# Optimization experiments

Hardware: AMD Instinct MI355X
Metric: run time of the kernel (lower is better)

## Reference

```python
import jax, jax.numpy as jnp
import numpy as np

B, C, P, L = 128, 5, 5, 5
D = 128
USER_NUM, TITLE_NUM, ENTITY_NUM, REL_NUM = 50000, 30000, 100000, 100


def setup_inputs() -> dict:
    key = jax.random.key(0)
    k = jax.random.split(key, 22)
    f = jnp.float32
    s = 0.1  # weight scale to keep LSTM gates in a sane range
    return {
        "candidate_newsindex": jax.random.randint(k[0], (B, C), 0, TITLE_NUM),
        "user_index": jax.random.randint(k[1], (B,), 0, USER_NUM),
        "total_paths_index": jax.random.randint(k[2], (USER_NUM, C, P, L), 0, TITLE_NUM),
        "total_type_index": jax.random.randint(k[3], (USER_NUM, C, P, L), 0, 3),
        "total_relations_index": jax.random.randint(k[4], (USER_NUM, C, P, L), 0, REL_NUM),
        "entity_emb": jax.random.normal(k[5], (ENTITY_NUM, D), f),
        "relation_emb": jax.random.normal(k[6], (REL_NUM, D), f),
        "user_emb": jax.random.normal(k[7], (USER_NUM, D), f),
        "news_emb": jax.random.normal(k[8], (TITLE_NUM, D), f),
        "type_emb": jax.random.normal(k[9], (3, D), f),
        "Wih0": jax.random.normal(k[10], (P, 4 * D, 3 * D), f) * s,
        "Whh0": jax.random.normal(k[11], (P, 4 * D, D), f) * s,
        "bih0": jax.random.normal(k[12], (P, 4 * D), f) * s,
        "bhh0": jax.random.normal(k[13], (P, 4 * D), f) * s,
        "Wih1": jax.random.normal(k[14], (P, 4 * D, D), f) * s,
        "Whh1": jax.random.normal(k[15], (P, 4 * D, D), f) * s,
        "bih1": jax.random.normal(k[16], (P, 4 * D), f) * s,
        "bhh1": jax.random.normal(k[17], (P, 4 * D), f) * s,
        "W1": jax.random.normal(k[18], (16, D), f) * s,
        "b1": jax.random.normal(k[19], (16,), f) * s,
        "W2": jax.random.normal(k[20], (1, 16), f) * s,
        "b2": jax.random.normal(k[21], (1,), f) * s,
    }


def _lstm2(x, Wih0, Whh0, bih0, bhh0, Wih1, Whh1, bih1, bhh1):
    """2-layer PyTorch-style LSTM (gate order i,f,g,o). x: [N, T, in] -> [N, T, H]."""
    def layer(x, Wih, Whh, bih, bhh):
        N = x.shape[0]
        H = Whh.shape[1]
        h0 = jnp.zeros((N, H), x.dtype)
        c0 = jnp.zeros((N, H), x.dtype)
        b = bih + bhh
        def step(carry, xt):
            h, c = carry
            g = xt @ Wih.T + h @ Whh.T + b
            i, f, gg, o = jnp.split(g, 4, axis=-1)
            c = jax.nn.sigmoid(f) * c + jax.nn.sigmoid(i) * jnp.tanh(gg)
            h = jax.nn.sigmoid(o) * jnp.tanh(c)
            return (h, c), h
        _, ys = jax.lax.scan(step, (h0, c0), x.swapaxes(0, 1))
        return ys.swapaxes(0, 1)
    x = layer(x, Wih0, Whh0, bih0, bhh0)
    x = layer(x, Wih1, Whh1, bih1, bhh1)
    return x


def reference(candidate_newsindex, user_index, total_paths_index, total_type_index,
              total_relations_index, entity_emb, relation_emb, user_emb, news_emb,
              type_emb, Wih0, Whh0, bih0, bhh0, Wih1, Whh1, bih1, bhh1,
              W1, b1, W2, b2):
    bpath = total_paths_index[user_index]  # [B,C,P,L]
    btype = total_type_index[user_index]
    brel = total_relations_index[user_index]
    # per-node embedding selected by type: 0->user, 1->news, else entity
    node = jnp.where((btype == 0)[..., None], user_emb[bpath],
                     jnp.where((btype == 1)[..., None], news_emb[bpath], entity_emb[bpath]))
    inp = jnp.concatenate([node, type_emb[btype], relation_emb[brel]], axis=-1)  # [B,C,P,L,3D]
    Bb, Cc, Pp, Ll, F = inp.shape
    x = inp.transpose(2, 0, 1, 3, 4).reshape(Pp, Bb * Cc, Ll, F)  # per-path batches
    outs = jax.vmap(_lstm2)(x, Wih0, Whh0, bih0, bhh0, Wih1, Whh1, bih1, bhh1)  # [P,BC,L,H]
    idx = jnp.arange(Pp)
    sel = outs[idx, :, idx, :]  # LSTM i's output at timestep i -> [P, BC, H]
    ps = jax.nn.sigmoid(jnp.maximum(sel @ W1.T + b1, 0.0) @ W2.T + b2)[..., 0]  # [P,BC]
    ps_mean = ps.reshape(Pp, Bb, Cc).mean(axis=0)  # [B,C]
    # faithful to source: total_output accumulates over candidates j, so the score
    # for candidate j is the cumulative mean of path scores for candidates 0..j
    total_score = jnp.cumsum(ps_mean, axis=1) / jnp.arange(1, Cc + 1, dtype=ps_mean.dtype)
    emb_score = jax.nn.sigmoid(jnp.sum(news_emb[candidate_newsindex] * user_emb[user_index][:, None, :], axis=-1))
    return emb_score + total_score
```

## Files before the change

kernel.cpp:

```cpp
#include <hip/hip_runtime.h>
#include <math.h>

#define BB   128
#define CC   5
#define PP   5
#define LL   5
#define DD   128
#define NSEQ 640
#define GATES 512
#define IN0  384
#define GSW  516
#define HPAD 136

typedef __attribute__((ext_vector_type(8))) short short8;
typedef __attribute__((ext_vector_type(4))) float f32x4;

__device__ __forceinline__ float sigf(float x){ return 1.0f/(1.0f+__expf(-x)); }
__device__ __forceinline__ float tanhfast(float x){ return 1.0f - 2.0f/(__expf(2.0f*x)+1.0f); }

__device__ __forceinline__ unsigned short f2bf(float x){
    union { float f; unsigned u; } v; v.f = x;
    unsigned r = v.u + 0x7FFF + ((v.u >> 16) & 1);
    return (unsigned short)(r >> 16);
}

__global__ void prep_kernel(const float* __restrict__ Wih0, const float* __restrict__ Whh0,
                            const float* __restrict__ Wih1, const float* __restrict__ Whh1,
                            const float* __restrict__ bih0, const float* __restrict__ bhh0,
                            const float* __restrict__ bih1, const float* __restrict__ bhh1,
                            unsigned short* __restrict__ F0, unsigned short* __restrict__ F1,
                            unsigned short* __restrict__ F2, unsigned short* __restrict__ F3,
                            float* __restrict__ b0, float* __restrict__ b1c){
    int id = blockIdx.x*256 + threadIdx.x;
    const int NF0 = PP*12*32*64;
    const int NFH = PP*4*32*64;
    if (id < NF0 + 3*NFH){
        const float* src; unsigned short* dst; int K, KT, fid;
        if (id < NF0){ src = Wih0; dst = F0; K = IN0; KT = 12; fid = id; }
        else {
            int j = id - NF0; int m = j / NFH; fid = j % NFH; K = DD; KT = 4;
            src = (m==0)?Whh0:(m==1)?Wih1:Whh1;
            dst = (m==0)?F1:(m==1)?F2:F3;
        }
        int lane = fid & 63; int rem = fid >> 6;
        int gt = rem & 31; rem >>= 5;
        int kt = rem % KT; int p = rem / KT;
        int g  = gt*16 + (lane & 15);
        int k0 = kt*32 + (lane >> 4)*8;
        const float* s = src + (size_t)(p*GATES + g)*K + k0;
        float4 x0 = *(const float4*)s;
        float4 x1 = *(const float4*)(s+4);
        uint4 o;
        o.x = f2bf(x0.x) | ((unsigned)f2bf(x0.y)<<16);
        o.y = f2bf(x0.z) | ((unsigned)f2bf(x0.w)<<16);
        o.z = f2bf(x1.x) | ((unsigned)f2bf(x1.y)<<16);
        o.w = f2bf(x1.z) | ((unsigned)f2bf(x1.w)<<16);
        *(uint4*)(dst + (size_t)fid*8) = o;
    } else {
        int j = id - (NF0 + 3*NFH);
        if (j < PP*GATES) b0[j] = bih0[j] + bhh0[j];
        else if (j < 2*PP*GATES){ int q = j - PP*GATES; b1c[q] = bih1[q] + bhh1[q]; }
    }
}

__global__ void gather_x(const int* __restrict__ user_index,
                         const int* __restrict__ tpath, const int* __restrict__ ttype,
                         const int* __restrict__ trel,
                         const float* __restrict__ entity_emb, const float* __restrict__ relation_emb,
                         const float* __restrict__ user_emb, const float* __restrict__ news_emb,
                         const float* __restrict__ type_emb,
                         unsigned short* __restrict__ X){
    int id = blockIdx.x*256 + threadIdx.x;
    if (id >= PP*LL*NSEQ*48) return;
    int pt = id / (NSEQ*48); int rem = id % (NSEQ*48);
    int n = rem / 48, q = rem % 48;
    int p = pt / LL, t = pt % LL;
    if (t > p) return;
    int b = n / CC, c = n % CC;
    int u = user_index[b];
    int base = ((u*CC + c)*PP + p)*LL + t;
    int col = q*8;
    const float* s;
    if (q < 16){
        int ty = ttype[base]; int pi = tpath[base];
        const float* e = (ty==0)?user_emb:(ty==1)?news_emb:entity_emb;
        s = e + (size_t)pi*DD + col;
    } else if (q < 32){
        s = type_emb + (size_t)ttype[base]*DD + (col-128);
    } else {
        s = relation_emb + (size_t)trel[base]*DD + (col-256);
    }
    float4 x0 = *(const float4*)s, x1 = *(const float4*)(s+4);
    uint4 o;
    o.x = f2bf(x0.x) | ((unsigned)f2bf(x0.y)<<16);
    o.y = f2bf(x0.z) | ((unsigned)f2bf(x0.w)<<16);
    o.z = f2bf(x1.x) | ((unsigned)f2bf(x1.y)<<16);
    o.w = f2bf(x1.z) | ((unsigned)f2bf(x1.w)<<16);
    *(uint4*)(X + (size_t)(pt*NSEQ + n)*IN0 + col) = o;
}

__global__ __launch_bounds__(256) void gemm_ih0_v3(const unsigned short* __restrict__ X,
                                                   const unsigned short* __restrict__ F0,
                                                   float* __restrict__ G0c){
    __shared__ unsigned short Bs[12*4*512];
    int bx = blockIdx.x;
    int nch = bx & 7;
    int m64 = (bx >> 3) % 10;
    int pt  = bx / 80;
    int p = pt / LL, t = pt % LL;
    if (t > p) return;
    int tid = threadIdx.x, lane = tid & 63, w = tid >> 6;
    int r16 = lane & 15, qd = lane >> 4;

    const unsigned short* Fp = F0 + (((size_t)p*12)*32 + nch*4)*512;
    uint4 breg[12];
    #pragma unroll
    for (int j=0;j<12;j++)
        breg[j] = *(const uint4*)(Fp + (size_t)j*32*512 + tid*8);
    #pragma unroll
    for (int j=0;j<12;j++)
        *(uint4*)(Bs + j*2048 + tid*8) = breg[j];
    __syncthreads();

    f32x4 acc[4];
    #pragma unroll
    for (int i=0;i<4;i++) acc[i] = (f32x4)0.0f;
    const unsigned short* Xb = X + ((size_t)pt*NSEQ + m64*64 + w*16 + r16)*IN0 + qd*8;
    #pragma unroll
    for (int kt=0; kt<12; kt++){
        short8 a = *(const short8*)(Xb + kt*32);
        #pragma unroll
        for (int i=0;i<4;i++){
            short8 bfr = *(const short8*)(Bs + (kt*4+i)*512 + lane*8);
            acc[i] = __builtin_amdgcn_mfma_f32_16x16x32_bf16(a, bfr, acc[i], 0,0,0);
        }
    }
    int tile16 = pt*40 + m64*4 + w;
    float* dst = G0c + (((size_t)tile16*32 + nch*4)*64 + lane)*4;
    #pragma unroll
    for (int i=0;i<4;i++)
        *(f32x4*)(dst + (size_t)i*256) = acc[i];
}

__global__ __launch_bounds__(512) void lstm_v3(
    const float* __restrict__ G0c,
    const unsigned short* __restrict__ F1,
    const unsigned short* __restrict__ F2,
    const unsigned short* __restrict__ F3,
    const float* __restrict__ b0, const float* __restrict__ b1c,
    const float* __restrict__ W1, const float* __restrict__ b1v,
    const float* __restrict__ W2, const float* __restrict__ b2v,
    float* __restrict__ psum){
    __shared__ float GS[16*GSW];
    __shared__ unsigned short h0T[16*HPAD];
    __shared__ unsigned short h1T[16*HPAD];
    __shared__ float h1f[16*132];
    __shared__ float mlpb[16*17];

    int p = blockIdx.x / 40, nt = blockIdx.x % 40;
    int n0 = nt*16;
    int tid = threadIdx.x;
    int lane = tid & 63, w = tid >> 6;
    int r16 = lane & 15, qd = lane >> 4;
    int cr = tid >> 5, cj = (tid & 31)*4;

    for (int i = tid; i < 16*HPAD/2; i += 512){
        ((unsigned*)h0T)[i] = 0u; ((unsigned*)h1T)[i] = 0u;
    }

    short8 f2r[16], f3r[16];
    {
        const unsigned short* F2p = F2 + (size_t)p*4*32*512 + lane*8;
        const unsigned short* F3p = F3 + (size_t)p*4*32*512 + lane*8;
        #pragma unroll
        for (int kt=0; kt<4; kt++)
            #pragma unroll
            for (int i=0;i<4;i++){
                f2r[kt*4+i] = *(const short8*)(F2p + (size_t)(kt*32 + w*4+i)*512);
                f3r[kt*4+i] = *(const short8*)(F3p + (size_t)(kt*32 + w*4+i)*512);
            }
    }
    float bL0[4], bL1[4];
    #pragma unroll
    for (int i=0;i<4;i++){
        int col = (w*4+i)*16 + r16;
        bL0[i] = b0[p*GATES + col];
        bL1[i] = b1c[p*GATES + col];
    }
    const unsigned short* F1p = F1 + (size_t)p*4*32*512 + lane*8;

    f32x4 pf[4];
    {
        const float* slab = G0c + (size_t)((p*LL + 0)*40 + nt)*8192;
        #pragma unroll
        for (int i=0;i<4;i++) pf[i] = *(const f32x4*)(slab + ((w*4+i)*64 + lane)*4);
    }
    float c0s[4] = {0,0,0,0}, c1s[4] = {0,0,0,0};
    __syncthreads();

    for (int t=0; t<=p; t++){
        f32x4 acc[4];
        #pragma unroll
        for (int i=0;i<4;i++){
            f32x4 a = pf[i]; float bb = bL0[i];
            a[0]+=bb; a[1]+=bb; a[2]+=bb; a[3]+=bb;
            acc[i] = a;
        }
        if (t < p){
            const float* ns = G0c + (size_t)((p*LL + t + 1)*40 + nt)*8192;
            #pragma unroll
            for (int i=0;i<4;i++) pf[i] = *(const f32x4*)(ns + ((w*4+i)*64 + lane)*4);
        }
        if (t > 0){
            #pragma unroll
            for (int kt=0; kt<4; kt++){
                short8 a = *(const short8*)(h0T + r16*HPAD + kt*32 + qd*8);
                #pragma unroll
                for (int i=0;i<4;i++){
                    short8 bfr = *(const short8*)(F1p + (size_t)(kt*32 + w*4+i)*512);
                    acc[i] = __builtin_amdgcn_mfma_f32_16x16x32_bf16(a, bfr, acc[i], 0,0,0);
                }
            }
        }
        #pragma unroll
        for (int i=0;i<4;i++)
            #pragma unroll
            for (int v=0;v<4;v++)
                GS[(qd*4+v)*GSW + (w*4+i)*16 + r16] = acc[i][v];
        __syncthreads();
        {
            const float* gsr = GS + cr*GSW;
            float4 gi = *(const float4*)(gsr + cj);
            float4 gf = *(const float4*)(gsr + 128 + cj);
            float4 gg = *(const float4*)(gsr + 256 + cj);
            float4 go = *(const float4*)(gsr + 384 + cj);
            float hv[4];
            const float* pi = (const float*)&gi; const float* pfv = (const float*)&gf;
            const float* pg = (const float*)&gg; const float* po = (const float*)&go;
            #pragma unroll
            for (int s=0;s<4;s++){
                float cc = sigf(pfv[s])*c0s[s] + sigf(pi[s])*tanhfast(pg[s]);
                c0s[s] = cc;
                hv[s] = sigf(po[s])*tanhfast(cc);
            }
            uint2 pk;
            pk.x = f2bf(hv[0]) | ((unsigned)f2bf(hv[1])<<16);
            pk.y = f2bf(hv[2]) | ((unsigned)f2bf(hv[3])<<16);
            *(uint2*)(h0T + cr*HPAD + cj) = pk;
        }
        __syncthreads();
        #pragma unroll
        for (int i=0;i<4;i++){
            float bb = bL1[i];
            f32x4 a; a[0]=bb; a[1]=bb; a[2]=bb; a[3]=bb;
            acc[i] = a;
        }
        #pragma unroll
        for (int kt=0; kt<4; kt++){
            short8 a = *(const short8*)(h0T + r16*HPAD + kt*32 + qd*8);
            #pragma unroll
            for (int i=0;i<4;i++)
                acc[i] = __builtin_amdgcn_mfma_f32_16x16x32_bf16(a, f2r[kt*4+i], acc[i], 0,0,0);
        }
        if (t > 0){
            #pragma unroll
            for (int kt=0; kt<4; kt++){
                short8 a = *(const short8*)(h1T + r16*HPAD + kt*32 + qd*8);
                #pragma unroll
                for (int i=0;i<4;i++)
                    acc[i] = __builtin_amdgcn_mfma_f32_16x16x32_bf16(a, f3r[kt*4+i], acc[i], 0,0,0);
            }
        }
        #pragma unroll
        for (int i=0;i<4;i++)
            #pragma unroll
            for (int v=0;v<4;v++)
                GS[(qd*4+v)*GSW + (w*4+i)*16 + r16] = acc[i][v];
        __syncthreads();
        {
            const float* gsr = GS + cr*GSW;
            float4 gi = *(const float4*)(gsr + cj);
            float4 gf = *(const float4*)(gsr + 128 + cj);
            float4 gg = *(const float4*)(gsr + 256 + cj);
            float4 go = *(const float4*)(gsr + 384 + cj);
            float hv[4];
            const float* pi = (const float*)&gi; const float* pfv = (const float*)&gf;
            const float* pg = (const float*)&gg; const float* po = (const float*)&go;
            #pragma unroll
            for (int s=0;s<4;s++){
                float cc = sigf(pfv[s])*c1s[s] + sigf(pi[s])*tanhfast(pg[s]);
                c1s[s] = cc;
                hv[s] = sigf(po[s])*tanhfast(cc);
            }
            if (t < p){
                uint2 pk;
                pk.x = f2bf(hv[0]) | ((unsigned)f2bf(hv[1])<<16);
                pk.y = f2bf(hv[2]) | ((unsigned)f2bf(hv[3])<<16);
                *(uint2*)(h1T + cr*HPAD + cj) = pk;
            } else {
                float4 st; st.x=hv[0]; st.y=hv[1]; st.z=hv[2]; st.w=hv[3];
                *(float4*)(h1f + cr*132 + cj) = st;
            }
        }
        __syncthreads();
    }
    if (tid < 256){
        int rr = tid & 15, hc = tid >> 4;
        const float* w1r = W1 + hc*DD;
        float acc = b1v[hc];
        #pragma unroll 4
        for (int k=0;k<DD;k++) acc = fmaf(h1f[rr*132 + k], w1r[k], acc);
        mlpb[hc*17 + rr] = fmaxf(acc, 0.0f);
    }
    __syncthreads();
    if (tid < 16){
        float s = b2v[0];
        #pragma unroll
        for (int h=0;h<16;h++) s = fmaf(mlpb[h*17 + tid], W2[h], s);
        atomicAdd(&psum[n0 + tid], 0.2f*sigf(s));
    }
}

__global__ void final_kernel(const int* __restrict__ cand, const int* __restrict__ user_index,
                             const float* __restrict__ news_emb, const float* __restrict__ user_emb,
                             const float* __restrict__ psum, float* __restrict__ out){
    int b = blockIdx.x;
    int lane = threadIdx.x;
    int u = user_index[b];
    const float* ue = user_emb + (size_t)u*DD;
    float cum = 0.0f;
    for (int c=0;c<CC;c++){
        int nb = cand[b*CC + c];
        const float* ne = news_emb + (size_t)nb*DD;
        float v = ne[lane]*ue[lane] + ne[lane+64]*ue[lane+64];
        #pragma unroll
        for (int off=32; off; off>>=1) v += __shfl_down(v, off, 64);
        if (lane == 0){
            cum += psum[b*CC + c];
            out[b*CC + c] = sigf(v) + cum/(float)(c+1);
        }
    }
}

extern "C" void kernel_launch(void* const* d_in, const int* in_sizes, int n_in,
                              void* d_out, int out_size, void* d_ws, size_t ws_size,
                              hipStream_t stream){
    const int* cand        = (const int*)d_in[0];
    const int* uidx        = (const int*)d_in[1];
    const int* tpath       = (const int*)d_in[2];
    const int* ttype       = (const int*)d_in[3];
    const int* trel        = (const int*)d_in[4];
    const float* entity_emb   = (const float*)d_in[5];
    const float* relation_emb = (const float*)d_in[6];
    const float* user_emb     = (const float*)d_in[7];
    const float* news_emb     = (const float*)d_in[8];
    const float* type_emb     = (const float*)d_in[9];
    const float* Wih0 = (const float*)d_in[10];
    const float* Whh0 = (const float*)d_in[11];
    const float* bih0 = (const float*)d_in[12];
    const float* bhh0 = (const float*)d_in[13];
    const float* Wih1 = (const float*)d_in[14];
    const float* Whh1 = (const float*)d_in[15];
    const float* bih1 = (const float*)d_in[16];
    const float* bhh1 = (const float*)d_in[17];
    const float* W1 = (const float*)d_in[18];
    const float* b1 = (const float*)d_in[19];
    const float* W2 = (const float*)d_in[20];
    const float* b2 = (const float*)d_in[21];
    float* out = (float*)d_out;

    char* ws = (char*)d_ws;
    unsigned short* F0 = (unsigned short*)ws;  ws += (size_t)PP*12*32*512*2;
    unsigned short* F1 = (unsigned short*)ws;  ws += (size_t)PP*4*32*512*2;
    unsigned short* F2 = (unsigned short*)ws;  ws += (size_t)PP*4*32*512*2;
    unsigned short* F3 = (unsigned short*)ws;  ws += (size_t)PP*4*32*512*2;
    float* b0  = (float*)ws;                   ws += PP*GATES*4;
    float* b1c = (float*)ws;                   ws += PP*GATES*4;
    unsigned short* X = (unsigned short*)ws;   ws += (size_t)PP*LL*NSEQ*IN0*2;
    float* G0c = (float*)ws;                   ws += (size_t)PP*LL*NSEQ*GATES*4;
    float* psum = (float*)ws;                  ws += NSEQ*4;

    hipMemsetAsync(psum, 0, NSEQ*sizeof(float), stream);
    prep_kernel<<<980,256,0,stream>>>(Wih0,Whh0,Wih1,Whh1,bih0,bhh0,bih1,bhh1,
                                      F0,F1,F2,F3,b0,b1c);
    gather_x<<<3000,256,0,stream>>>(uidx,tpath,ttype,trel,entity_emb,relation_emb,
                                    user_emb,news_emb,type_emb,X);
    gemm_ih0_v3<<<2000,256,0,stream>>>(X, F0, G0c);
    lstm_v3<<<200,512,0,stream>>>(G0c, F1, F2, F3, b0, b1c, W1, b1, W2, b2, psum);
    final_kernel<<<BB,64,0,stream>>>(cand, uidx, news_emb, user_emb, psum, out);
}
```

Before: 240.0 us.

## Fuse layer-0 input GEMM into LSTM kernel and compute gates in registers

Drops the separate gemm_ih0 kernel and its fp32 G0c intermediate. The LSTM kernel now runs the X·Wih0 MFMAs itself at each timestep, reading F0 fragments straight from global/L2. The gate columns are remapped (i*8+w) so each thread holds the i,f,g,o values for the same hidden unit in its accumulators. That removes the shared-memory gate staging buffer and one barrier per layer step. The psum memset is also folded into prep_kernel, saving a launch. The cost is extra serial MFMA work and global weight loads inside the 200-block recurrent kernel, which has low occupancy.

```diff
diff --git a/kernel.cpp b/kernel.cpp
--- a/kernel.cpp
+++ b/kernel.cpp
@@ -9,7 +9,6 @@
 #define NSEQ 640
 #define GATES 512
 #define IN0  384
-#define GSW  516
 #define HPAD 136
 
 typedef __attribute__((ext_vector_type(8))) short short8;
@@ -30,7 +29,8 @@
                             const float* __restrict__ bih1, const float* __restrict__ bhh1,
                             unsigned short* __restrict__ F0, unsigned short* __restrict__ F1,
                             unsigned short* __restrict__ F2, unsigned short* __restrict__ F3,
-                            float* __restrict__ b0, float* __restrict__ b1c){
+                            float* __restrict__ b0, float* __restrict__ b1c,
+                            float* __restrict__ psum){
     int id = blockIdx.x*256 + threadIdx.x;
     const int NF0 = PP*12*32*64;
     const int NFH = PP*4*32*64;
@@ -60,6 +60,7 @@
         int j = id - (NF0 + 3*NFH);
         if (j < PP*GATES) b0[j] = bih0[j] + bhh0[j];
         else if (j < 2*PP*GATES){ int q = j - PP*GATES; b1c[q] = bih1[q] + bhh1[q]; }
+        else if (j < 2*PP*GATES + NSEQ){ psum[j - 2*PP*GATES] = 0.0f; }
     }
 }
 
@@ -99,51 +100,9 @@
     *(uint4*)(X + (size_t)(pt*NSEQ + n)*IN0 + col) = o;
 }
 
-__global__ __launch_bounds__(256) void gemm_ih0_v3(const unsigned short* __restrict__ X,
-                                                   const unsigned short* __restrict__ F0,
-                                                   float* __restrict__ G0c){
-    __shared__ unsigned short Bs[12*4*512];
-    int bx = blockIdx.x;
-    int nch = bx & 7;
-    int m64 = (bx >> 3) % 10;
-    int pt  = bx / 80;
-    int p = pt / LL, t = pt % LL;
-    if (t > p) return;
-    int tid = threadIdx.x, lane = tid & 63, w = tid >> 6;
-    int r16 = lane & 15, qd = lane >> 4;
-
-    const unsigned short* Fp = F0 + (((size_t)p*12)*32 + nch*4)*512;
-    uint4 breg[12];
-    #pragma unroll
-    for (int j=0;j<12;j++)
-        breg[j] = *(const uint4*)(Fp + (size_t)j*32*512 + tid*8);
-    #pragma unroll
-    for (int j=0;j<12;j++)
-        *(uint4*)(Bs + j*2048 + tid*8) = breg[j];
-    __syncthreads();
-
-    f32x4 acc[4];
-    #pragma unroll
-    for (int i=0;i<4;i++) acc[i] = (f32x4)0.0f;
-    const unsigned short* Xb = X + ((size_t)pt*NSEQ + m64*64 + w*16 + r16)*IN0 + qd*8;
-    #pragma unroll
-    for (int kt=0; kt<12; kt++){
-        short8 a = *(const short8*)(Xb + kt*32);
-        #pragma unroll
-        for (int i=0;i<4;i++){
-            short8 bfr = *(const short8*)(Bs + (kt*4+i)*512 + lane*8);
-            acc[i] = __builtin_amdgcn_mfma_f32_16x16x32_bf16(a, bfr, acc[i], 0,0,0);
-        }
-    }
-    int tile16 = pt*40 + m64*4 + w;
-    float* dst = G0c + (((size_t)tile16*32 + nch*4)*64 + lane)*4;
-    #pragma unroll
-    for (int i=0;i<4;i++)
-        *(f32x4*)(dst + (size_t)i*256) = acc[i];
-}
-
-__global__ __launch_bounds__(512) void lstm_v3(
-    const float* __restrict__ G0c,
+__global__ __launch_bounds__(512) void lstm_v4(
+    const unsigned short* __restrict__ X,
+    const unsigned short* __restrict__ F0,
     const unsigned short* __restrict__ F1,
     const unsigned short* __restrict__ F2,
     const unsigned short* __restrict__ F3,
@@ -151,7 +110,6 @@
     const float* __restrict__ W1, const float* __restrict__ b1v,
     const float* __restrict__ W2, const float* __restrict__ b2v,
     float* __restrict__ psum){
-    __shared__ float GS[16*GSW];
     __shared__ unsigned short h0T[16*HPAD];
     __shared__ unsigned short h1T[16*HPAD];
     __shared__ float h1f[16*132];
@@ -162,11 +120,7 @@
     int tid = threadIdx.x;
     int lane = tid & 63, w = tid >> 6;
     int r16 = lane & 15, qd = lane >> 4;
-    int cr = tid >> 5, cj = (tid & 31)*4;
-
-    for (int i = tid; i < 16*HPAD/2; i += 512){
-        ((unsigned*)h0T)[i] = 0u; ((unsigned*)h1T)[i] = 0u;
-    }
+    int j = w*16 + r16;
 
     short8 f2r[16], f3r[16];
     {
@@ -176,40 +130,38 @@
         for (int kt=0; kt<4; kt++)
             #pragma unroll
             for (int i=0;i<4;i++){
-                f2r[kt*4+i] = *(const short8*)(F2p + (size_t)(kt*32 + w*4+i)*512);
-                f3r[kt*4+i] = *(const short8*)(F3p + (size_t)(kt*32 + w*4+i)*512);
+                f2r[kt*4+i] = *(const short8*)(F2p + (size_t)(kt*32 + i*8 + w)*512);
+                f3r[kt*4+i] = *(const short8*)(F3p + (size_t)(kt*32 + i*8 + w)*512);
             }
     }
     float bL0[4], bL1[4];
     #pragma unroll
     for (int i=0;i<4;i++){
-        int col = (w*4+i)*16 + r16;
+        int col = (i*8 + w)*16 + r16;
         bL0[i] = b0[p*GATES + col];
         bL1[i] = b1c[p*GATES + col];
     }
+    const unsigned short* F0p = F0 + (size_t)p*12*32*512 + lane*8;
     const unsigned short* F1p = F1 + (size_t)p*4*32*512 + lane*8;
 
-    f32x4 pf[4];
-    {
-        const float* slab = G0c + (size_t)((p*LL + 0)*40 + nt)*8192;
-        #pragma unroll
-        for (int i=0;i<4;i++) pf[i] = *(const f32x4*)(slab + ((w*4+i)*64 + lane)*4);
-    }
     float c0s[4] = {0,0,0,0}, c1s[4] = {0,0,0,0};
-    __syncthreads();
 
     for (int t=0; t<=p; t++){
         f32x4 acc[4];
         #pragma unroll
         for (int i=0;i<4;i++){
-            f32x4 a = pf[i]; float bb = bL0[i];
-            a[0]+=bb; a[1]+=bb; a[2]+=bb; a[3]+=bb;
-            acc[i] = a;
-        }
-        if (t < p){
-            const float* ns = G0c + (size_t)((p*LL + t + 1)*40 + nt)*8192;
-            #pragma unroll
-            for (int i=0;i<4;i++) pf[i] = *(const f32x4*)(ns + ((w*4+i)*64 + lane)*4);
+            float bb = bL0[i];
+            f32x4 a; a[0]=bb; a[1]=bb; a[2]=bb; a[3]=bb; acc[i]=a;
+        }
+        const unsigned short* Xb = X + ((size_t)((p*LL+t)*NSEQ) + n0 + r16)*IN0 + qd*8;
+        #pragma unroll
+        for (int kt=0; kt<12; kt++){
+            short8 a = *(const short8*)(Xb + kt*32);
+            #pragma unroll
+            for (int i=0;i<4;i++){
+                short8 bfr = *(const short8*)(F0p + (size_t)(kt*32 + i*8 + w)*512);
+                acc[i] = __builtin_amdgcn_mfma_f32_16x16x32_bf16(a, bfr, acc[i], 0,0,0);
+            }
         }
         if (t > 0){
             #pragma unroll
@@ -217,43 +169,23 @@
                 short8 a = *(const short8*)(h0T + r16*HPAD + kt*32 + qd*8);
                 #pragma unroll
                 for (int i=0;i<4;i++){
-                    short8 bfr = *(const short8*)(F1p + (size_t)(kt*32 + w*4+i)*512);
+                    short8 bfr = *(const short8*)(F1p + (size_t)(kt*32 + i*8 + w)*512);
                     acc[i] = __builtin_amdgcn_mfma_f32_16x16x32_bf16(a, bfr, acc[i], 0,0,0);
                 }
             }
         }
-        #pragma unroll
-        for (int i=0;i<4;i++)
-            #pragma unroll
-            for (int v=0;v<4;v++)
-                GS[(qd*4+v)*GSW + (w*4+i)*16 + r16] = acc[i][v];
         __syncthreads();
-        {
-            const float* gsr = GS + cr*GSW;
-            float4 gi = *(const float4*)(gsr + cj);
-            float4 gf = *(const float4*)(gsr + 128 + cj);
-            float4 gg = *(const float4*)(gsr + 256 + cj);
-            float4 go = *(const float4*)(gsr + 384 + cj);
-            float hv[4];
-            const float* pi = (const float*)&gi; const float* pfv = (const float*)&gf;
-            const float* pg = (const float*)&gg; const float* po = (const float*)&go;
-            #pragma unroll
-            for (int s=0;s<4;s++){
-                float cc = sigf(pfv[s])*c0s[s] + sigf(pi[s])*tanhfast(pg[s]);
-                c0s[s] = cc;
-                hv[s] = sigf(po[s])*tanhfast(cc);
-            }
-            uint2 pk;
-            pk.x = f2bf(hv[0]) | ((unsigned)f2bf(hv[1])<<16);
-            pk.y = f2bf(hv[2]) | ((unsigned)f2bf(hv[3])<<16);
-            *(uint2*)(h0T + cr*HPAD + cj) = pk;
+        #pragma unroll
+        for (int v=0; v<4; v++){
+            float cc = sigf(acc[1][v])*c0s[v] + sigf(acc[0][v])*tanhfast(acc[2][v]);
+            c0s[v] = cc;
+            h0T[(qd*4+v)*HPAD + j] = f2bf(sigf(acc[3][v])*tanhfast(cc));
         }
         __syncthreads();
         #pragma unroll
         for (int i=0;i<4;i++){
             float bb = bL1[i];
-            f32x4 a; a[0]=bb; a[1]=bb; a[2]=bb; a[3]=bb;
-            acc[i] = a;
+            f32x4 a; a[0]=bb; a[1]=bb; a[2]=bb; a[3]=bb; acc[i]=a;
         }
         #pragma unroll
         for (int kt=0; kt<4; kt++){
@@ -271,39 +203,17 @@
                     acc[i] = __builtin_amdgcn_mfma_f32_16x16x32_bf16(a, f3r[kt*4+i], acc[i], 0,0,0);
             }
         }
-        #pragma unroll
-        for (int i=0;i<4;i++)
-            #pragma unroll
-            for (int v=0;v<4;v++)
-                GS[(qd*4+v)*GSW + (w*4+i)*16 + r16] = acc[i][v];
         __syncthreads();
-        {
-            const float* gsr = GS + cr*GSW;
-            float4 gi = *(const float4*)(gsr + cj);
-            float4 gf = *(const float4*)(gsr + 128 + cj);
-            float4 gg = *(const float4*)(gsr + 256 + cj);
-            float4 go = *(const float4*)(gsr + 384 + cj);
-            float hv[4];
-            const float* pi = (const float*)&gi; const float* pfv = (const float*)&gf;
-            const float* pg = (const float*)&gg; const float* po = (const float*)&go;
-            #pragma unroll
-            for (int s=0;s<4;s++){
-                float cc = sigf(pfv[s])*c1s[s] + sigf(pi[s])*tanhfast(pg[s]);
-                c1s[s] = cc;
-                hv[s] = sigf(po[s])*tanhfast(cc);
-            }
-            if (t < p){
-                uint2 pk;
-                pk.x = f2bf(hv[0]) | ((unsigned)f2bf(hv[1])<<16);
-                pk.y = f2bf(hv[2]) | ((unsigned)f2bf(hv[3])<<16);
-                *(uint2*)(h1T + cr*HPAD + cj) = pk;
-            } else {
-                float4 st; st.x=hv[0]; st.y=hv[1]; st.z=hv[2]; st.w=hv[3];
-                *(float4*)(h1f + cr*132 + cj) = st;
-            }
-        }
-        __syncthreads();
-    }
+        #pragma unroll
+        for (int v=0; v<4; v++){
+            float cc = sigf(acc[1][v])*c1s[v] + sigf(acc[0][v])*tanhfast(acc[2][v]);
+            c1s[v] = cc;
+            float hh = sigf(acc[3][v])*tanhfast(cc);
+            if (t < p) h1T[(qd*4+v)*HPAD + j] = f2bf(hh);
+            else       h1f[(qd*4+v)*132 + j] = hh;
+        }
+    }
+    __syncthreads();
     if (tid < 256){
         int rr = tid & 15, hc = tid >> 4;
         const float* w1r = W1 + hc*DD;
@@ -377,15 +287,12 @@
     float* b0  = (float*)ws;                   ws += PP*GATES*4;
     float* b1c = (float*)ws;                   ws += PP*GATES*4;
     unsigned short* X = (unsigned short*)ws;   ws += (size_t)PP*LL*NSEQ*IN0*2;
-    float* G0c = (float*)ws;                   ws += (size_t)PP*LL*NSEQ*GATES*4;
     float* psum = (float*)ws;                  ws += NSEQ*4;
 
-    hipMemsetAsync(psum, 0, NSEQ*sizeof(float), stream);
-    prep_kernel<<<980,256,0,stream>>>(Wih0,Whh0,Wih1,Whh1,bih0,bhh0,bih1,bhh1,
-                                      F0,F1,F2,F3,b0,b1c);
+    prep_kernel<<<985,256,0,stream>>>(Wih0,Whh0,Wih1,Whh1,bih0,bhh0,bih1,bhh1,
+                                      F0,F1,F2,F3,b0,b1c,psum);
     gather_x<<<3000,256,0,stream>>>(uidx,tpath,ttype,trel,entity_emb,relation_emb,
                                     user_emb,news_emb,type_emb,X);
-    gemm_ih0_v3<<<2000,256,0,stream>>>(X, F0, G0c);
-    lstm_v3<<<200,512,0,stream>>>(G0c, F1, F2, F3, b0, b1c, W1, b1, W2, b2, psum);
+    lstm_v4<<<200,512,0,stream>>>(X, F0, F1, F2, F3, b0, b1c, W1, b1, W2, b2, psum);
     final_kernel<<<BB,64,0,stream>>>(cand, uidx, news_emb, user_emb, psum, out);
 }
```

Measured after the change: 299.3 us. +24.7%, slower.
